# Kernel tuning notes

Hardware: AMD Instinct MI355X
Metric: run time of the kernel (lower is better)

The kernel has to match this reference:

```python
import jax, jax.numpy as jnp
import numpy as np

N = 1024        # batch of tokens (module is per-token; we vmap via batched einsums)
IN = 1024       # in_features
H = 16          # num_heads
D = 64          # head_dim
BD = 512        # binary_dim
M = 8192        # num memories
OUT = H * D     # out_features
TEMP = 0.01
EPS = 1e-5


def setup_inputs() -> dict:
    key = jax.random.key(0)
    ks = jax.random.split(key, 8)
    return {
        "x": jax.random.normal(ks[0], (N, IN), jnp.float32),
        "Wq": jax.random.normal(ks[1], (OUT, IN), jnp.float32) / np.sqrt(IN).astype(np.float32),
        "bq_bias": jax.random.normal(ks[2], (OUT,), jnp.float32) * 0.01,
        "bin_proj": jax.random.normal(ks[3], (H, BD, D), jnp.float32),
        "bin_inv": jax.random.normal(ks[4], (H, D, BD), jnp.float32) / np.float32(BD),
        # binary memory codes in {-1, +1}
        "weight_matrix": jnp.sign(jax.random.normal(ks[5], (H, M, BD), jnp.float32)),
        "ln_w": jnp.ones((OUT,), jnp.float32),
        "ln_b": jnp.zeros((OUT,), jnp.float32),
    }


def reference(x, Wq, bq_bias, bin_proj, bin_inv, weight_matrix, ln_w, ln_b):
    # query projection: [N, OUT] -> [N, H, D], L2-normalize per head
    q = (x @ Wq.T + bq_bias).reshape(N, H, D)
    q = q / jnp.linalg.norm(q, axis=-1, keepdims=True)
    # sign-encode into binary space: [N, H, BD]
    code = jnp.sign(jnp.einsum('nhd,hbd->nhb', q, bin_proj))
    # cosine-transformed Hamming-similarity scores: [N, H, M]
    sim = jnp.einsum('nhb,hmb->nhm', code, weight_matrix) / np.float32(BD)
    scores = jnp.cos((np.float32(np.pi) / 2) * (1.0 - sim))
    attn = jax.nn.softmax(scores / np.float32(TEMP), axis=-1)
    # readout from binary memories, project back to real space
    out = jnp.einsum('nhm,hmb->nhb', attn, weight_matrix)
    out = jnp.einsum('nhb,hdb->nhd', out, bin_inv)
    out = out / jnp.linalg.norm(out, axis=-1, keepdims=True)
    out = out.reshape(N, OUT)
    # LayerNorm over out_features
    mu = jnp.mean(out, axis=-1, keepdims=True)
    var = jnp.var(out, axis=-1, keepdims=True)
    return (out - mu) / jnp.sqrt(var + np.float32(EPS)) * ln_w + ln_b
```

## Files before the change

### kernel.cpp

```cpp
#include <hip/hip_runtime.h>
#include <hip/hip_fp16.h>

#define NTOK 1024
#define INF  1024
#define NH   16
#define DH   64
#define BDIM 512
#define NMEM 8192
#define OUTF 1024
#define NWRD 16

typedef _Float16 f16x8 __attribute__((ext_vector_type(8)));
typedef float    f32x4 __attribute__((ext_vector_type(4)));
typedef int      i32x4 __attribute__((ext_vector_type(4)));

#define GLOAD16(G, L) __builtin_amdgcn_global_load_lds( \
    (const __attribute__((address_space(1))) unsigned int*)(G), \
    (__attribute__((address_space(3))) unsigned int*)(L), 16, 0, 0)

__device__ inline float score2(float s) {
  return 144.2695040889f * __sinf(s * 0.0030679615757712823f);
}

__global__ __launch_bounds__(256) void k_qgemm(const float* __restrict__ x,
    const float* __restrict__ Wq, const float* __restrict__ bq, float* __restrict__ q) {
  __shared__ float As[64][17];
  __shared__ float Bs[64][17];
  const int tx = threadIdx.x & 15, ty = threadIdx.x >> 4;
  const int n0 = blockIdx.y * 64, o0 = blockIdx.x * 64;
  const int r = threadIdx.x >> 2, c4 = (threadIdx.x & 3) * 4;
  float acc[4][4] = {};
  for (int k0 = 0; k0 < INF; k0 += 16) {
    float4 av = *(const float4*)&x[(size_t)(n0 + r) * INF + k0 + c4];
    float4 bv = *(const float4*)&Wq[(size_t)(o0 + r) * INF + k0 + c4];
    __syncthreads();
    As[r][c4+0] = av.x; As[r][c4+1] = av.y; As[r][c4+2] = av.z; As[r][c4+3] = av.w;
    Bs[r][c4+0] = bv.x; Bs[r][c4+1] = bv.y; Bs[r][c4+2] = bv.z; Bs[r][c4+3] = bv.w;
    __syncthreads();
    #pragma unroll
    for (int kk = 0; kk < 16; ++kk) {
      float a[4], b[4];
      #pragma unroll
      for (int i = 0; i < 4; ++i) a[i] = As[ty*4+i][kk];
      #pragma unroll
      for (int j = 0; j < 4; ++j) b[j] = Bs[tx*4+j][kk];
      #pragma unroll
      for (int i = 0; i < 4; ++i)
        #pragma unroll
        for (int j = 0; j < 4; ++j) acc[i][j] += a[i] * b[j];
    }
  }
  #pragma unroll
  for (int i = 0; i < 4; ++i) {
    const int row = n0 + ty*4 + i;
    #pragma unroll
    for (int j = 0; j < 4; ++j) {
      const int col = o0 + tx*4 + j;
      q[(size_t)row * OUTF + col] = acc[i][j] + bq[col];
    }
  }
}

__global__ __launch_bounds__(256) void k_code(const float* __restrict__ q,
    const float* __restrict__ bp, signed char* __restrict__ code_i8) {
  const int h = blockIdx.y, n0 = blockIdx.x * 16;
  __shared__ float ql[16][68];
  const int t = threadIdx.x;
  {
    const int r = t >> 4, c = (t & 15) * 4;
    float4 v = *(const float4*)&q[(size_t)(n0 + r) * OUTF + h * 64 + c];
    ql[r][c] = v.x; ql[r][c+1] = v.y; ql[r][c+2] = v.z; ql[r][c+3] = v.w;
  }
  __syncthreads();
  #pragma unroll
  for (int bb = 0; bb < 512; bb += 256) {
    const int b = bb + t;
    float bpv[64];
    const float4* src = (const float4*)&bp[((size_t)h * BDIM + b) * 64];
    #pragma unroll
    for (int j = 0; j < 16; ++j) {
      float4 v = src[j];
      bpv[j*4] = v.x; bpv[j*4+1] = v.y; bpv[j*4+2] = v.z; bpv[j*4+3] = v.w;
    }
    for (int n = 0; n < 16; ++n) {
      float dot = 0.f;
      #pragma unroll
      for (int d = 0; d < 64; ++d) dot += bpv[d] * ql[n][d];
      code_i8[((size_t)h * NTOK + n0 + n) * BDIM + b] = dot > 0.f ? 1 : -1;
    }
  }
}

__global__ __launch_bounds__(256) void k_packw(const float* __restrict__ w,
    unsigned* __restrict__ wp, signed char* __restrict__ w_i8) {
  const int row  = blockIdx.x * 4 + (threadIdx.x >> 6);
  const int lane = threadIdx.x & 63;
  const float* src = w + (size_t)row * BDIM;
  unsigned my = 0;
  #pragma unroll
  for (int kk = 0; kk < 8; ++kk) {
    float v = src[kk * 64 + lane];
    const int c = kk * 4 + (lane >> 4);
    const int p = (c & ~7) | ((c & 7) ^ (row & 7));
    w_i8[(size_t)row * BDIM + p * 16 + (lane & 15)] = v > 0.f ? 1 : -1;
    unsigned long long m = __ballot(v > 0.f);
    if ((lane >> 1) == kk) my = (lane & 1) ? (unsigned)(m >> 32) : (unsigned)m;
  }
  if (lane < 16) wp[(size_t)row * NWRD + lane] = my;
}

__global__ __launch_bounds__(256) void k_binT(const float* __restrict__ binv,
                                              float* __restrict__ bT) {
  const int h = blockIdx.y, b0 = blockIdx.x * 64;
  __shared__ float tl[64][65];
  const int t = threadIdx.x;
  #pragma unroll
  for (int i = 0; i < 4; ++i) {
    int fi = t + 256 * i;
    int d = fi >> 4, b = (fi & 15) * 4;
    float4 v = *(const float4*)&binv[((size_t)h * DH + d) * BDIM + b0 + b];
    tl[d][b] = v.x; tl[d][b+1] = v.y; tl[d][b+2] = v.z; tl[d][b+3] = v.w;
  }
  __syncthreads();
  #pragma unroll
  for (int i = 0; i < 4; ++i) {
    int fo = t + 256 * i;
    int bb = fo >> 4, dd = (fo & 15) * 4;
    float4 v = { tl[dd][bb], tl[dd+1][bb], tl[dd+2][bb], tl[dd+3][bb] };
    *(float4*)&bT[((size_t)h * BDIM + b0 + bb) * DH + dd] = v;
  }
}

__global__ __launch_bounds__(256) void k_wt(const unsigned* __restrict__ wp,
    unsigned short* __restrict__ wt, int h0) {
  const int hg = blockIdx.z, h = h0 + hg;
  const int b0 = blockIdx.y * 64, m0 = blockIdx.x * 256;
  __shared__ unsigned bits[256][2];
  const int t = threadIdx.x;
  const unsigned* src = wp + (size_t)(h * NMEM + m0 + t) * NWRD + (b0 >> 5);
  bits[t][0] = src[0]; bits[t][1] = src[1];
  __syncthreads();
  const int b = t >> 2, ms = (t & 3) * 64;
  const int wd = b >> 5, sh = b & 31;
  const int bx7 = b & 7;
  unsigned short* dst = wt + ((size_t)hg * BDIM + b0 + b) * NMEM + m0 + ms;
  #pragma unroll
  for (int g = 0; g < 8; ++g) {
    const int pg = g ^ bx7;
    const int j = ms + g * 8;
    ushort4 v0, v1;
    v0.x = ((bits[j+0][wd] >> sh) & 1) ? 0x3C00 : 0xBC00;
    v0.y = ((bits[j+1][wd] >> sh) & 1) ? 0x3C00 : 0xBC00;
    v0.z = ((bits[j+2][wd] >> sh) & 1) ? 0x3C00 : 0xBC00;
    v0.w = ((bits[j+3][wd] >> sh) & 1) ? 0x3C00 : 0xBC00;
    v1.x = ((bits[j+4][wd] >> sh) & 1) ? 0x3C00 : 0xBC00;
    v1.y = ((bits[j+5][wd] >> sh) & 1) ? 0x3C00 : 0xBC00;
    v1.z = ((bits[j+6][wd] >> sh) & 1) ? 0x3C00 : 0xBC00;
    v1.w = ((bits[j+7][wd] >> sh) & 1) ? 0x3C00 : 0xBC00;
    *(ushort4*)&dst[pg * 8]     = v0;
    *(ushort4*)&dst[pg * 8 + 4] = v1;
  }
}

__global__ __launch_bounds__(512, 2) void k_sim(const signed char* __restrict__ code_i8,
    const signed char* __restrict__ w_i8, unsigned short* __restrict__ attn,
    int h0, int gmask, int gshift) {
  const int bid = (int)blockIdx.x;
  const int hg = bid & gmask, h = h0 + hg;
  const int n0 = (bid >> gshift) * 32;
  const int t = threadIdx.x, lane = t & 63, wid = t >> 6;
  __shared__ __align__(16) signed char Bls[128 * 512];
  __shared__ __align__(16) _Float16 Pls[32][136];
  __shared__ int smaxl[32];
  if (t < 32) smaxl[t] = -(1 << 30);
  const int rg = wid >> 2, mg = wid & 3;
  i32x4 afrag[8];
  #pragma unroll
  for (int kk = 0; kk < 8; ++kk)
    afrag[kk] = *(const i32x4*)(code_i8 +
        ((size_t)h * NTOK + n0 + rg * 16 + (lane & 15)) * BDIM +
        kk * 64 + (lane >> 4) * 16);
  const signed char* wb = w_i8 + (size_t)h * NMEM * BDIM + (size_t)t * 16;
  signed char* const d0 = &Bls[wid * 1024];
  int vmax[4] = {-(1 << 30), -(1 << 30), -(1 << 30), -(1 << 30)};
  for (int tile = 0; tile < 64; ++tile) {
    const signed char* s = wb + (size_t)tile * 128 * BDIM;
    __syncthreads();
    #pragma unroll
    for (int seg = 0; seg < 8; ++seg)
      GLOAD16(s + seg * 8192, d0 + seg * 8192);
    __syncthreads();
    #pragma unroll
    for (int msub = 0; msub < 2; ++msub) {
      const signed char* bls = &Bls[(mg * 32 + msub * 16 + (lane & 15)) * 512];
      i32x4 acc = {};
      #pragma unroll
      for (int kk = 0; kk < 8; ++kk) {
        const int c = kk * 4 + (lane >> 4);
        const int p = (c & ~7) | ((c & 7) ^ (lane & 7));
        i32x4 b = *(const i32x4*)(bls + p * 16);
        acc = __builtin_amdgcn_mfma_i32_16x16x64_i8(afrag[kk], b, acc, 0, 0, 0);
      }
      #pragma unroll
      for (int j = 0; j < 4; ++j) vmax[j] = max(vmax[j], acc[j]);
    }
  }
  #pragma unroll
  for (int j = 0; j < 4; ++j) {
    int v = vmax[j];
    #pragma unroll
    for (int s = 1; s < 16; s <<= 1) v = max(v, __shfl_xor(v, s));
    if ((lane & 15) == 0)
      atomicMax(&smaxl[rg * 16 + (lane >> 4) * 4 + j], v);
  }
  __syncthreads();
  float sm[4];
  #pragma unroll
  for (int j = 0; j < 4; ++j)
    sm[j] = score2((float)smaxl[rg * 16 + (lane >> 4) * 4 + j]);
  const int srow = t >> 4, sg = t & 15;
  unsigned short* const sdst = attn + ((size_t)hg * NTOK + n0 + srow) * NMEM;
  const int spc = ((sg & 7) ^ (srow & 7)) * 8 + (sg >> 3) * 64;
  for (int tile = 0; tile < 64; ++tile) {
    const signed char* s = wb + (size_t)tile * 128 * BDIM;
    __syncthreads();
    #pragma unroll
    for (int seg = 0; seg < 8; ++seg)
      GLOAD16(s + seg * 8192, d0 + seg * 8192);
    if (tile > 0) {
      f16x8 pv = *(const f16x8*)&Pls[srow][sg * 8];
      *(f16x8*)(sdst + (size_t)(tile - 1) * 128 + spc) = pv;
    }
    __syncthreads();
    #pragma unroll
    for (int msub = 0; msub < 2; ++msub) {
      const signed char* bls = &Bls[(mg * 32 + msub * 16 + (lane & 15)) * 512];
      i32x4 acc = {};
      #pragma unroll
      for (int kk = 0; kk < 8; ++kk) {
        const int c = kk * 4 + (lane >> 4);
        const int p = (c & ~7) | ((c & 7) ^ (lane & 7));
        i32x4 b = *(const i32x4*)(bls + p * 16);
        acc = __builtin_amdgcn_mfma_i32_16x16x64_i8(afrag[kk], b, acc, 0, 0, 0);
      }
      const int col = mg * 32 + msub * 16 + (lane & 15);
      #pragma unroll
      for (int j = 0; j < 4; ++j) {
        const int r0 = rg * 16 + (lane >> 4) * 4 + j;
        float pr = exp2f(score2((float)acc[j]) - sm[j]);
        Pls[r0][col] = (_Float16)pr;
      }
    }
  }
  __syncthreads();
  {
    f16x8 pv = *(const f16x8*)&Pls[srow][sg * 8];
    *(f16x8*)(sdst + (size_t)63 * 128 + spc) = pv;
  }
}

__global__ __launch_bounds__(512, 2) void k_stageF(const unsigned short* __restrict__ attn,
    const unsigned short* __restrict__ wt, float* __restrict__ o1t,
    int gmask, int gshift) {
  __shared__ __align__(16) _Float16 Al[128][64];
  __shared__ __align__(16) _Float16 Bl[128][64];
  const int wg = (int)blockIdx.x;
  const int hg = wg & gmask;
  const int rest = wg >> gshift;
  const int nt = rest & 7, bt = rest >> 3;
  const int n0 = nt * 128, b0 = bt * 128;
  const int t = threadIdx.x;
  const int lane = t & 63, wid = t >> 6;
  const int wm = wid >> 2, wn = wid & 3;
  f32x4 acc[4][2];
  #pragma unroll
  for (int i = 0; i < 4; ++i)
    #pragma unroll
    for (int j = 0; j < 2; ++j) acc[i][j] = (f32x4){0.f, 0.f, 0.f, 0.f};

  const unsigned short* ag = attn + ((size_t)hg * NTOK + n0 + 16*wid + (lane >> 3)) * NMEM + (lane & 7) * 8;
  const unsigned short* bg = wt   + ((size_t)hg * BDIM + b0 + 16*wid + (lane >> 3)) * NMEM + (lane & 7) * 8;
  _Float16* al0 = &Al[16 * wid][0];
  _Float16* bl0 = &Bl[16 * wid][0];

  for (int k0 = 0; k0 < NMEM; k0 += 64) {
    __syncthreads();
    GLOAD16(ag + k0,            al0);
    GLOAD16(ag + k0 + 8 * NMEM, al0 + 8 * 64);
    GLOAD16(bg + k0,            bl0);
    GLOAD16(bg + k0 + 8 * NMEM, bl0 + 8 * 64);
    __syncthreads();
    #pragma unroll
    for (int kk = 0; kk < 64; kk += 32) {
      const int phys = (((kk >> 3) + (lane >> 4)) ^ (lane & 7)) * 8;
      f16x8 af[4], bf[2];
      #pragma unroll
      for (int fm = 0; fm < 4; ++fm)
        af[fm] = *(const f16x8*)&Al[wm*64 + fm*16 + (lane & 15)][phys];
      #pragma unroll
      for (int fn = 0; fn < 2; ++fn)
        bf[fn] = *(const f16x8*)&Bl[wn*32 + fn*16 + (lane & 15)][phys];
      #pragma unroll
      for (int fm = 0; fm < 4; ++fm)
        #pragma unroll
        for (int fn = 0; fn < 2; ++fn)
          acc[fm][fn] = __builtin_amdgcn_mfma_f32_16x16x32_f16(af[fm], bf[fn], acc[fm][fn], 0, 0, 0);
    }
  }
  #pragma unroll
  for (int fm = 0; fm < 4; ++fm) {
    const int rowb = n0 + wm*64 + fm*16 + (lane >> 4) * 4;
    #pragma unroll
    for (int fn = 0; fn < 2; ++fn) {
      const int col = b0 + wn*32 + fn*16 + (lane & 15);
      *(f32x4*)&o1t[((size_t)hg * BDIM + col) * NTOK + rowb] = acc[fm][fn];
    }
  }
}

__global__ __launch_bounds__(256) void k_proj(const float* __restrict__ o1t,
    const float* __restrict__ bT, float* __restrict__ o2, int h0) {
  const int hg = blockIdx.y, h = h0 + hg;
  const int n0 = blockIdx.x * 64;
  __shared__ float bl[128][68];
  __shared__ float ol[128][68];
  __shared__ float outl[64][68];
  __shared__ float nrm[64];
  const int t = threadIdx.x;
  const int tx = t & 15, ty = t >> 4;
  float acc[4][4] = {};
  for (int c = 0; c < 4; ++c) {
    const int bb0 = c * 128;
    __syncthreads();
    #pragma unroll
    for (int i = 0; i < 8; ++i) {
      int fi = t + 256 * i;
      int rr = fi >> 4, cc = (fi & 15) * 4;
      *(float4*)&bl[rr][cc] = *(const float4*)&bT[((size_t)h * BDIM + bb0 + rr) * DH + cc];
      *(float4*)&ol[rr][cc] = *(const float4*)&o1t[((size_t)hg * BDIM + bb0 + rr) * NTOK + n0 + cc];
    }
    __syncthreads();
    for (int bb = 0; bb < 128; ++bb) {
      float4 bd = *(const float4*)&bl[bb][tx * 4];
      float4 on = *(const float4*)&ol[bb][ty * 4];
      float ai[4] = {on.x, on.y, on.z, on.w};
      float bj[4] = {bd.x, bd.y, bd.z, bd.w};
      #pragma unroll
      for (int i = 0; i < 4; ++i)
        #pragma unroll
        for (int j = 0; j < 4; ++j) acc[i][j] += ai[i] * bj[j];
    }
  }
  __syncthreads();
  #pragma unroll
  for (int i = 0; i < 4; ++i)
    #pragma unroll
    for (int j = 0; j < 4; ++j) outl[ty*4 + i][tx*4 + j] = acc[i][j];
  __syncthreads();
  if (t < 64) {
    float s = 0.f;
    #pragma unroll
    for (int d = 0; d < 64; ++d) { float v = outl[t][d]; s += v * v; }
    nrm[t] = 1.f / sqrtf(s);
  }
  __syncthreads();
  {
    const int n = t >> 2, dg = (t & 3) * 16;
    #pragma unroll
    for (int j = 0; j < 16; ++j)
      o2[(size_t)(n0 + n) * OUTF + h * 64 + dg + j] = outl[n][dg + j] * nrm[n];
  }
}

__global__ __launch_bounds__(256) void k_ln(const float* __restrict__ o2,
    const float* __restrict__ lnw, const float* __restrict__ lnb, float* __restrict__ out) {
  const int n = blockIdx.x, t = threadIdx.x;
  __shared__ float red[4];
  float4 v = *(const float4*)&o2[(size_t)n * OUTF + t * 4];
  float s = v.x + v.y + v.z + v.w;
  const int lane = t & 63, wid = t >> 6;
  #pragma unroll
  for (int off = 32; off; off >>= 1) s += __shfl_down(s, off);
  if (lane == 0) red[wid] = s;
  __syncthreads();
  const float mu = (red[0] + red[1] + red[2] + red[3]) * (1.f / 1024.f);
  float4 d = {v.x - mu, v.y - mu, v.z - mu, v.w - mu};
  float s2 = d.x*d.x + d.y*d.y + d.z*d.z + d.w*d.w;
  #pragma unroll
  for (int off = 32; off; off >>= 1) s2 += __shfl_down(s2, off);
  __syncthreads();
  if (lane == 0) red[wid] = s2;
  __syncthreads();
  const float var = (red[0] + red[1] + red[2] + red[3]) * (1.f / 1024.f);
  const float inv = 1.f / sqrtf(var + 1e-5f);
  float4 w = *(const float4*)&lnw[t * 4];
  float4 b = *(const float4*)&lnb[t * 4];
  float4 o = { d.x*inv*w.x + b.x, d.y*inv*w.y + b.y,
               d.z*inv*w.z + b.z, d.w*inv*w.w + b.w };
  *(float4*)&out[(size_t)n * OUTF + t * 4] = o;
}

extern "C" void kernel_launch(void* const* d_in, const int* in_sizes, int n_in,
                              void* d_out, int out_size, void* d_ws, size_t ws_size,
                              hipStream_t stream) {
  (void)in_sizes; (void)n_in; (void)out_size;
  const float* x    = (const float*)d_in[0];
  const float* Wq   = (const float*)d_in[1];
  const float* bq   = (const float*)d_in[2];
  const float* bp   = (const float*)d_in[3];
  const float* binv = (const float*)d_in[4];
  const float* wm   = (const float*)d_in[5];
  const float* lnw  = (const float*)d_in[6];
  const float* lnb  = (const float*)d_in[7];
  float* outp = (float*)d_out;

  char* ws = (char*)d_ws;
  size_t off = 0;
  auto carve = [&](size_t bytes) -> char* {
    char* p = ws + off;
    off += (bytes + 255) & ~(size_t)255;
    return p;
  };
  float*       q       = (float*)      carve((size_t)NTOK * OUTF * 4);
  signed char* code_i8 = (signed char*)carve((size_t)NH * NTOK * BDIM);
  unsigned*    wpk     = (unsigned*)   carve((size_t)NH * NMEM * NWRD * 4);
  signed char* w_i8    = (signed char*)carve((size_t)NH * NMEM * BDIM);
  float*       bT      = (float*)      carve((size_t)NH * BDIM * DH * 4);
  float*       o2      = (float*)      carve((size_t)NTOK * OUTF * 4);
  const size_t fixed = off;
  const size_t per = ((size_t)BDIM * NMEM * 2 + 256)
                   + ((size_t)NTOK * NMEM * 2 + 256)
                   + ((size_t)BDIM * NTOK * 4 + 256);
  int G = 16;
  while (G > 1 && fixed + (size_t)G * per > ws_size) G >>= 1;
  unsigned short* wt   = (unsigned short*)carve((size_t)G * BDIM * NMEM * 2);
  unsigned short* attn = (unsigned short*)carve((size_t)G * NTOK * NMEM * 2);
  float*          o1t  = (float*)         carve((size_t)G * BDIM * NTOK * 4);
  const int gshift = __builtin_ctz(G);

  k_qgemm<<<dim3(16, 16), 256, 0, stream>>>(x, Wq, bq, q);
  k_code <<<dim3(64, 16), 256, 0, stream>>>(q, bp, code_i8);
  k_packw<<<dim3(NH * NMEM / 4), 256, 0, stream>>>(wm, wpk, w_i8);
  k_binT <<<dim3(8, 16), 256, 0, stream>>>(binv, bT);
  for (int h0 = 0; h0 < NH; h0 += G) {
    k_wt    <<<dim3(32, 8, G), 256, 0, stream>>>(wpk, wt, h0);
    k_sim   <<<dim3(32 * G),   512, 0, stream>>>(code_i8, w_i8, attn, h0, G - 1, gshift);
    k_stageF<<<dim3(32 * G),   512, 0, stream>>>(attn, wt, o1t, G - 1, gshift);
    k_proj  <<<dim3(16, G),    256, 0, stream>>>(o1t, bT, o2, h0);
  }
  k_ln<<<dim3(NTOK), 256, 0, stream>>>(o2, lnw, lnb, outp);
}
```

Baseline: 738.3 us.

## Widen k_sim row tile to 64 tokens per block, reuse each B fragment across four MFMAs

k_sim now gives each block 64 token rows instead of 32, and each of the 8 waves owns 16 memory columns across all 64 rows. Each B fragment read from LDS now feeds four MFMAs instead of one. This halves the number of blocks, so each streamed weight tile is used for twice as many tokens. In exchange, the A-fragment register footprint grows fourfold, which could spill or lower occupancy under launch_bounds(512,2). The grid is also halved, leaving fewer blocks to fill the CUs.

```diff
diff --git a/kernel.cpp b/kernel.cpp
--- a/kernel.cpp
+++ b/kernel.cpp
@@ -167,22 +167,28 @@
     int h0, int gmask, int gshift) {
   const int bid = (int)blockIdx.x;
   const int hg = bid & gmask, h = h0 + hg;
-  const int n0 = (bid >> gshift) * 32;
-  const int t = threadIdx.x, lane = t & 63, wid = t >> 6;
+  const int n0 = (bid >> gshift) * 64;
+  const int t = threadIdx.x, lane = t & 63, mg = t >> 6;
   __shared__ __align__(16) signed char Bls[128 * 512];
-  __shared__ __align__(16) _Float16 Pls[32][136];
-  __shared__ int smaxl[32];
-  if (t < 32) smaxl[t] = -(1 << 30);
-  const int rg = wid >> 2, mg = wid & 3;
-  i32x4 afrag[8];
-  #pragma unroll
-  for (int kk = 0; kk < 8; ++kk)
-    afrag[kk] = *(const i32x4*)(code_i8 +
-        ((size_t)h * NTOK + n0 + rg * 16 + (lane & 15)) * BDIM +
-        kk * 64 + (lane >> 4) * 16);
+  __shared__ __align__(16) _Float16 Pls[64][136];
+  __shared__ int smaxl[64];
+  if (t < 64) smaxl[t] = -(1 << 30);
+  i32x4 afrag[4][8];
+  #pragma unroll
+  for (int fi = 0; fi < 4; ++fi)
+    #pragma unroll
+    for (int kk = 0; kk < 8; ++kk)
+      afrag[fi][kk] = *(const i32x4*)(code_i8 +
+          ((size_t)h * NTOK + n0 + fi * 16 + (lane & 15)) * BDIM +
+          kk * 64 + (lane >> 4) * 16);
   const signed char* wb = w_i8 + (size_t)h * NMEM * BDIM + (size_t)t * 16;
-  signed char* const d0 = &Bls[wid * 1024];
-  int vmax[4] = {-(1 << 30), -(1 << 30), -(1 << 30), -(1 << 30)};
+  signed char* const d0 = &Bls[mg * 1024];
+  const signed char* const bls = &Bls[(mg * 16 + (lane & 15)) * 512];
+  int vmax[4][4];
+  #pragma unroll
+  for (int fi = 0; fi < 4; ++fi)
+    #pragma unroll
+    for (int j = 0; j < 4; ++j) vmax[fi][j] = -(1 << 30);
   for (int tile = 0; tile < 64; ++tile) {
     const signed char* s = wb + (size_t)tile * 128 * BDIM;
     __syncthreads();
@@ -190,37 +196,41 @@
     for (int seg = 0; seg < 8; ++seg)
       GLOAD16(s + seg * 8192, d0 + seg * 8192);
     __syncthreads();
-    #pragma unroll
-    for (int msub = 0; msub < 2; ++msub) {
-      const signed char* bls = &Bls[(mg * 32 + msub * 16 + (lane & 15)) * 512];
-      i32x4 acc = {};
-      #pragma unroll
-      for (int kk = 0; kk < 8; ++kk) {
-        const int c = kk * 4 + (lane >> 4);
-        const int p = (c & ~7) | ((c & 7) ^ (lane & 7));
-        i32x4 b = *(const i32x4*)(bls + p * 16);
-        acc = __builtin_amdgcn_mfma_i32_16x16x64_i8(afrag[kk], b, acc, 0, 0, 0);
-      }
-      #pragma unroll
-      for (int j = 0; j < 4; ++j) vmax[j] = max(vmax[j], acc[j]);
-    }
-  }
-  #pragma unroll
-  for (int j = 0; j < 4; ++j) {
-    int v = vmax[j];
-    #pragma unroll
-    for (int s = 1; s < 16; s <<= 1) v = max(v, __shfl_xor(v, s));
-    if ((lane & 15) == 0)
-      atomicMax(&smaxl[rg * 16 + (lane >> 4) * 4 + j], v);
-  }
-  __syncthreads();
-  float sm[4];
-  #pragma unroll
-  for (int j = 0; j < 4; ++j)
-    sm[j] = score2((float)smaxl[rg * 16 + (lane >> 4) * 4 + j]);
-  const int srow = t >> 4, sg = t & 15;
+    i32x4 acc[4] = {};
+    #pragma unroll
+    for (int kk = 0; kk < 8; ++kk) {
+      const int c = kk * 4 + (lane >> 4);
+      const int p = (c & ~7) | ((c & 7) ^ (lane & 7));
+      i32x4 b = *(const i32x4*)(bls + p * 16);
+      #pragma unroll
+      for (int fi = 0; fi < 4; ++fi)
+        acc[fi] = __builtin_amdgcn_mfma_i32_16x16x64_i8(afrag[fi][kk], b, acc[fi], 0, 0, 0);
+    }
+    #pragma unroll
+    for (int fi = 0; fi < 4; ++fi)
+      #pragma unroll
+      for (int j = 0; j < 4; ++j) vmax[fi][j] = max(vmax[fi][j], acc[fi][j]);
+  }
+  #pragma unroll
+  for (int fi = 0; fi < 4; ++fi)
+    #pragma unroll
+    for (int j = 0; j < 4; ++j) {
+      int v = vmax[fi][j];
+      #pragma unroll
+      for (int s = 1; s < 16; s <<= 1) v = max(v, __shfl_xor(v, s));
+      if ((lane & 15) == 0)
+        atomicMax(&smaxl[fi * 16 + (lane >> 4) * 4 + j], v);
+    }
+  __syncthreads();
+  float sm[4][4];
+  #pragma unroll
+  for (int fi = 0; fi < 4; ++fi)
+    #pragma unroll
+    for (int j = 0; j < 4; ++j)
+      sm[fi][j] = score2((float)smaxl[fi * 16 + (lane >> 4) * 4 + j]);
+  const int srow = t >> 3, sg = t & 7;
   unsigned short* const sdst = attn + ((size_t)hg * NTOK + n0 + srow) * NMEM;
-  const int spc = ((sg & 7) ^ (srow & 7)) * 8 + (sg >> 3) * 64;
+  const int sp1 = (sg ^ (srow & 7)) * 8;
   for (int tile = 0; tile < 64; ++tile) {
     const signed char* s = wb + (size_t)tile * 128 * BDIM;
     __syncthreads();
@@ -228,34 +238,38 @@
     for (int seg = 0; seg < 8; ++seg)
       GLOAD16(s + seg * 8192, d0 + seg * 8192);
     if (tile > 0) {
-      f16x8 pv = *(const f16x8*)&Pls[srow][sg * 8];
-      *(f16x8*)(sdst + (size_t)(tile - 1) * 128 + spc) = pv;
-    }
-    __syncthreads();
-    #pragma unroll
-    for (int msub = 0; msub < 2; ++msub) {
-      const signed char* bls = &Bls[(mg * 32 + msub * 16 + (lane & 15)) * 512];
-      i32x4 acc = {};
-      #pragma unroll
-      for (int kk = 0; kk < 8; ++kk) {
-        const int c = kk * 4 + (lane >> 4);
-        const int p = (c & ~7) | ((c & 7) ^ (lane & 7));
-        i32x4 b = *(const i32x4*)(bls + p * 16);
-        acc = __builtin_amdgcn_mfma_i32_16x16x64_i8(afrag[kk], b, acc, 0, 0, 0);
-      }
-      const int col = mg * 32 + msub * 16 + (lane & 15);
+      f16x8 pv0 = *(const f16x8*)&Pls[srow][sg * 8];
+      f16x8 pv1 = *(const f16x8*)&Pls[srow][64 + sg * 8];
+      *(f16x8*)(sdst + (size_t)(tile - 1) * 128 + sp1)      = pv0;
+      *(f16x8*)(sdst + (size_t)(tile - 1) * 128 + 64 + sp1) = pv1;
+    }
+    __syncthreads();
+    i32x4 acc[4] = {};
+    #pragma unroll
+    for (int kk = 0; kk < 8; ++kk) {
+      const int c = kk * 4 + (lane >> 4);
+      const int p = (c & ~7) | ((c & 7) ^ (lane & 7));
+      i32x4 b = *(const i32x4*)(bls + p * 16);
+      #pragma unroll
+      for (int fi = 0; fi < 4; ++fi)
+        acc[fi] = __builtin_amdgcn_mfma_i32_16x16x64_i8(afrag[fi][kk], b, acc[fi], 0, 0, 0);
+    }
+    const int col = mg * 16 + (lane & 15);
+    #pragma unroll
+    for (int fi = 0; fi < 4; ++fi)
       #pragma unroll
       for (int j = 0; j < 4; ++j) {
-        const int r0 = rg * 16 + (lane >> 4) * 4 + j;
-        float pr = exp2f(score2((float)acc[j]) - sm[j]);
+        const int r0 = fi * 16 + (lane >> 4) * 4 + j;
+        float pr = exp2f(score2((float)acc[fi][j]) - sm[fi][j]);
         Pls[r0][col] = (_Float16)pr;
       }
-    }
   }
   __syncthreads();
   {
-    f16x8 pv = *(const f16x8*)&Pls[srow][sg * 8];
-    *(f16x8*)(sdst + (size_t)63 * 128 + spc) = pv;
+    f16x8 pv0 = *(const f16x8*)&Pls[srow][sg * 8];
+    f16x8 pv1 = *(const f16x8*)&Pls[srow][64 + sg * 8];
+    *(f16x8*)(sdst + (size_t)63 * 128 + sp1)      = pv0;
+    *(f16x8*)(sdst + (size_t)63 * 128 + 64 + sp1) = pv1;
   }
 }
 
@@ -444,7 +458,7 @@
   k_binT <<<dim3(8, 16), 256, 0, stream>>>(binv, bT);
   for (int h0 = 0; h0 < NH; h0 += G) {
     k_wt    <<<dim3(32, 8, G), 256, 0, stream>>>(wpk, wt, h0);
-    k_sim   <<<dim3(32 * G),   512, 0, stream>>>(code_i8, w_i8, attn, h0, G - 1, gshift);
+    k_sim   <<<dim3(16 * G),   512, 0, stream>>>(code_i8, w_i8, attn, h0, G - 1, gshift);
     k_stageF<<<dim3(32 * G),   512, 0, stream>>>(attn, wt, o1t, G - 1, gshift);
     k_proj  <<<dim3(16, G),    256, 0, stream>>>(o1t, bT, o2, h0);
   }
```

New measurement: 775.6 us. +5.1%, slower.

## Feed stageF B operand from transposed bitmasks via LDS lookup table

Applied to the files above, without the earlier changes.

Drops the fp16 ±1 transposed memory matrix (wt) and its per-group k_wt kernel. A one-time kernel now builds a bit-packed transposed mask (64 memories per uint64), and stageF expands each byte into an f16x8 MFMA fragment through a 256-entry LDS lookup table. This cuts the global traffic for the B operand by about 16x and removes a large workspace buffer, which may also allow a larger head-group G. The cost is per-iteration 64-bit global loads issued by each lane plus LUT reads that can hit LDS bank conflicts.

```diff
diff --git a/kernel.cpp b/kernel.cpp
--- a/kernel.cpp
+++ b/kernel.cpp
@@ -109,6 +109,24 @@
   if (lane < 16) wp[(size_t)row * NWRD + lane] = my;
 }
 
+__global__ __launch_bounds__(256) void k_wtb(const unsigned* __restrict__ wp,
+    unsigned long long* __restrict__ wtb) {
+  const int h = blockIdx.y;
+  const int mg = blockIdx.x;
+  const int lane = threadIdx.x & 63, wv = threadIdx.x >> 6;
+  const int m = mg * 64 + lane;
+  #pragma unroll
+  for (int wi = 0; wi < 4; ++wi) {
+    const int wd = wv * 4 + wi;
+    const unsigned word = wp[(size_t)(h * NMEM + m) * NWRD + wd];
+    for (int j = 0; j < 32; ++j) {
+      unsigned long long msk = __ballot((word >> j) & 1);
+      if (lane == 0)
+        wtb[((size_t)h * BDIM + wd * 32 + j) * 128 + mg] = msk;
+    }
+  }
+}
+
 __global__ __launch_bounds__(256) void k_binT(const float* __restrict__ binv,
                                               float* __restrict__ bT) {
   const int h = blockIdx.y, b0 = blockIdx.x * 64;
@@ -128,37 +146,6 @@
     int bb = fo >> 4, dd = (fo & 15) * 4;
     float4 v = { tl[dd][bb], tl[dd+1][bb], tl[dd+2][bb], tl[dd+3][bb] };
     *(float4*)&bT[((size_t)h * BDIM + b0 + bb) * DH + dd] = v;
-  }
-}
-
-__global__ __launch_bounds__(256) void k_wt(const unsigned* __restrict__ wp,
-    unsigned short* __restrict__ wt, int h0) {
-  const int hg = blockIdx.z, h = h0 + hg;
-  const int b0 = blockIdx.y * 64, m0 = blockIdx.x * 256;
-  __shared__ unsigned bits[256][2];
-  const int t = threadIdx.x;
-  const unsigned* src = wp + (size_t)(h * NMEM + m0 + t) * NWRD + (b0 >> 5);
-  bits[t][0] = src[0]; bits[t][1] = src[1];
-  __syncthreads();
-  const int b = t >> 2, ms = (t & 3) * 64;
-  const int wd = b >> 5, sh = b & 31;
-  const int bx7 = b & 7;
-  unsigned short* dst = wt + ((size_t)hg * BDIM + b0 + b) * NMEM + m0 + ms;
-  #pragma unroll
-  for (int g = 0; g < 8; ++g) {
-    const int pg = g ^ bx7;
-    const int j = ms + g * 8;
-    ushort4 v0, v1;
-    v0.x = ((bits[j+0][wd] >> sh) & 1) ? 0x3C00 : 0xBC00;
-    v0.y = ((bits[j+1][wd] >> sh) & 1) ? 0x3C00 : 0xBC00;
-    v0.z = ((bits[j+2][wd] >> sh) & 1) ? 0x3C00 : 0xBC00;
-    v0.w = ((bits[j+3][wd] >> sh) & 1) ? 0x3C00 : 0xBC00;
-    v1.x = ((bits[j+4][wd] >> sh) & 1) ? 0x3C00 : 0xBC00;
-    v1.y = ((bits[j+5][wd] >> sh) & 1) ? 0x3C00 : 0xBC00;
-    v1.z = ((bits[j+6][wd] >> sh) & 1) ? 0x3C00 : 0xBC00;
-    v1.w = ((bits[j+7][wd] >> sh) & 1) ? 0x3C00 : 0xBC00;
-    *(ushort4*)&dst[pg * 8]     = v0;
-    *(ushort4*)&dst[pg * 8 + 4] = v1;
   }
 }
 
@@ -260,16 +247,21 @@
 }
 
 __global__ __launch_bounds__(512, 2) void k_stageF(const unsigned short* __restrict__ attn,
-    const unsigned short* __restrict__ wt, float* __restrict__ o1t,
+    const unsigned long long* __restrict__ wtb, float* __restrict__ o1t,
     int gmask, int gshift) {
   __shared__ __align__(16) _Float16 Al[128][64];
-  __shared__ __align__(16) _Float16 Bl[128][64];
+  __shared__ __align__(16) _Float16 lut[256][8];
+  const int t = threadIdx.x;
+  if (t < 256) {
+    #pragma unroll
+    for (int j = 0; j < 8; ++j)
+      lut[t][j] = ((t >> j) & 1) ? (_Float16)1.f : (_Float16)-1.f;
+  }
   const int wg = (int)blockIdx.x;
   const int hg = wg & gmask;
   const int rest = wg >> gshift;
   const int nt = rest & 7, bt = rest >> 3;
   const int n0 = nt * 128, b0 = bt * 128;
-  const int t = threadIdx.x;
   const int lane = t & 63, wid = t >> 6;
   const int wm = wid >> 2, wn = wid & 3;
   f32x4 acc[4][2];
@@ -279,27 +271,27 @@
     for (int j = 0; j < 2; ++j) acc[i][j] = (f32x4){0.f, 0.f, 0.f, 0.f};
 
   const unsigned short* ag = attn + ((size_t)hg * NTOK + n0 + 16*wid + (lane >> 3)) * NMEM + (lane & 7) * 8;
-  const unsigned short* bg = wt   + ((size_t)hg * BDIM + b0 + 16*wid + (lane >> 3)) * NMEM + (lane & 7) * 8;
   _Float16* al0 = &Al[16 * wid][0];
-  _Float16* bl0 = &Bl[16 * wid][0];
+  const unsigned long long* wb0 = wtb + ((size_t)hg * BDIM + b0 + wn * 32 + (lane & 15)) * 128;
+  const unsigned long long* wb1 = wb0 + 16 * 128;
 
   for (int k0 = 0; k0 < NMEM; k0 += 64) {
+    const unsigned long long bits0 = wb0[k0 >> 6];
+    const unsigned long long bits1 = wb1[k0 >> 6];
     __syncthreads();
     GLOAD16(ag + k0,            al0);
     GLOAD16(ag + k0 + 8 * NMEM, al0 + 8 * 64);
-    GLOAD16(bg + k0,            bl0);
-    GLOAD16(bg + k0 + 8 * NMEM, bl0 + 8 * 64);
     __syncthreads();
     #pragma unroll
     for (int kk = 0; kk < 64; kk += 32) {
       const int phys = (((kk >> 3) + (lane >> 4)) ^ (lane & 7)) * 8;
+      const int sh = kk + (lane >> 4) * 8;
       f16x8 af[4], bf[2];
       #pragma unroll
       for (int fm = 0; fm < 4; ++fm)
         af[fm] = *(const f16x8*)&Al[wm*64 + fm*16 + (lane & 15)][phys];
-      #pragma unroll
-      for (int fn = 0; fn < 2; ++fn)
-        bf[fn] = *(const f16x8*)&Bl[wn*32 + fn*16 + (lane & 15)][phys];
+      bf[0] = *(const f16x8*)&lut[(unsigned)(bits0 >> sh) & 0xFFu][0];
+      bf[1] = *(const f16x8*)&lut[(unsigned)(bits1 >> sh) & 0xFFu][0];
       #pragma unroll
       for (int fm = 0; fm < 4; ++fm)
         #pragma unroll
@@ -425,15 +417,14 @@
   signed char* code_i8 = (signed char*)carve((size_t)NH * NTOK * BDIM);
   unsigned*    wpk     = (unsigned*)   carve((size_t)NH * NMEM * NWRD * 4);
   signed char* w_i8    = (signed char*)carve((size_t)NH * NMEM * BDIM);
+  unsigned long long* wtb = (unsigned long long*)carve((size_t)NH * BDIM * 128 * 8);
   float*       bT      = (float*)      carve((size_t)NH * BDIM * DH * 4);
   float*       o2      = (float*)      carve((size_t)NTOK * OUTF * 4);
   const size_t fixed = off;
-  const size_t per = ((size_t)BDIM * NMEM * 2 + 256)
-                   + ((size_t)NTOK * NMEM * 2 + 256)
+  const size_t per = ((size_t)NTOK * NMEM * 2 + 256)
                    + ((size_t)BDIM * NTOK * 4 + 256);
   int G = 16;
   while (G > 1 && fixed + (size_t)G * per > ws_size) G >>= 1;
-  unsigned short* wt   = (unsigned short*)carve((size_t)G * BDIM * NMEM * 2);
   unsigned short* attn = (unsigned short*)carve((size_t)G * NTOK * NMEM * 2);
   float*          o1t  = (float*)         carve((size_t)G * BDIM * NTOK * 4);
   const int gshift = __builtin_ctz(G);
@@ -441,11 +432,11 @@
   k_qgemm<<<dim3(16, 16), 256, 0, stream>>>(x, Wq, bq, q);
   k_code <<<dim3(64, 16), 256, 0, stream>>>(q, bp, code_i8);
   k_packw<<<dim3(NH * NMEM / 4), 256, 0, stream>>>(wm, wpk, w_i8);
+  k_wtb  <<<dim3(128, NH), 256, 0, stream>>>(wpk, wtb);
   k_binT <<<dim3(8, 16), 256, 0, stream>>>(binv, bT);
   for (int h0 = 0; h0 < NH; h0 += G) {
-    k_wt    <<<dim3(32, 8, G), 256, 0, stream>>>(wpk, wt, h0);
     k_sim   <<<dim3(32 * G),   512, 0, stream>>>(code_i8, w_i8, attn, h0, G - 1, gshift);
-    k_stageF<<<dim3(32 * G),   512, 0, stream>>>(attn, wt, o1t, G - 1, gshift);
+    k_stageF<<<dim3(32 * G),   512, 0, stream>>>(attn, wtb + (size_t)h0 * BDIM * 128, o1t, G - 1, gshift);
     k_proj  <<<dim3(16, G),    256, 0, stream>>>(o1t, bT, o2, h0);
   }
   k_ln<<<dim3(NTOK), 256, 0, stream>>>(o2, lnw, lnb, outp);
```

Measured after the change: 708.3 us. -4.1%, faster.
